# Kernel optimization log

Measured on AMD Instinct MI355X. Metric: run time of the kernel, lower is better.

The kernel has to match this reference:

```python
import jax, jax.numpy as jnp
import numpy as np

N_GRAPHS = 512
NODES_PER_G = 200
EDGES_PER_G = 6400
N = N_GRAPHS * NODES_PER_G        # 102400 nodes
E = N_GRAPHS * EDGES_PER_G        # 3276800 edges
HID = 128
NCLS = 10


def _linear_params(key, fan_in, fan_out):
    # torch nn.Linear default init: U(-1/sqrt(fan_in), 1/sqrt(fan_in))
    s = 1.0 / np.sqrt(fan_in)
    kw, kb = jax.random.split(key)
    W = jax.random.uniform(kw, (fan_in, fan_out), minval=-s, maxval=s, dtype=jnp.float32)
    b = jax.random.uniform(kb, (fan_out,), minval=-s, maxval=s, dtype=jnp.float32)
    return W, b


def setup_inputs() -> dict:
    key = jax.random.key(0)
    ks = jax.random.split(key, 10)
    # edges are confined within each graph (DGL batched graph structure)
    g_off = (jnp.arange(E, dtype=jnp.int32) // EDGES_PER_G) * NODES_PER_G
    src = (g_off + jax.random.randint(ks[0], (E,), 0, NODES_PER_G)).astype(jnp.int32)
    dst = (g_off + jax.random.randint(ks[1], (E,), 0, NODES_PER_G)).astype(jnp.int32)
    W1, b1 = _linear_params(ks[2], 1, HID)
    W2, b2 = _linear_params(ks[3], HID, HID)
    Wa, ba = _linear_params(ks[4], HID, 512)
    Wb, bb = _linear_params(ks[5], 512, 1024)
    Wc, bc = _linear_params(ks[6], 1024, 1024)
    Wd, bd = _linear_params(ks[7], 1024, 512)
    We, be = _linear_params(ks[8], 512, NCLS)
    return dict(src=src, dst=dst, W1=W1, b1=b1, W2=W2, b2=b2,
                Wa=Wa, ba=ba, Wb=Wb, bb=bb, Wc=Wc, bc=bc,
                Wd=Wd, bd=bd, We=We, be=be)


def reference(src, dst, W1, b1, W2, b2, Wa, ba, Wb, bb, Wc, bc, Wd, bd, We, be):
    seg = jax.ops.segment_sum
    ones = jnp.ones((E,), jnp.float32)
    in_deg = seg(ones, dst, num_segments=N)    # [N]
    out_deg = seg(ones, src, num_segments=N)   # [N]
    # DGL GraphConv norm='both': degrees clamped to min 1
    inv_out = (1.0 / jnp.sqrt(jnp.maximum(out_deg, 1.0)))[:, None]
    inv_in = (1.0 / jnp.sqrt(jnp.maximum(in_deg, 1.0)))[:, None]

    def gconv(h, W, b):
        h = (h @ W) * inv_out                    # src-side normalize (weight applied first; same math)
        h = seg(h[src], dst, num_segments=N)     # gather + scatter-add aggregation
        return h * inv_in + b                    # dst-side normalize + bias

    h = in_deg[:, None]                          # input node features = in-degrees, [N,1]
    h = jax.nn.relu(gconv(h, W1, b1))
    h = jax.nn.relu(gconv(h, W2, b2))

    gid = jnp.arange(N, dtype=jnp.int32) // NODES_PER_G
    hg = seg(h, gid, num_segments=N_GRAPHS) / float(NODES_PER_G)  # mean readout, [G,HID]

    x = jax.nn.relu(hg @ Wa + ba)
    x = jax.nn.relu(x @ Wb + bb)
    x = jax.nn.relu(x @ Wc + bc)
    x = jax.nn.relu(x @ Wd + bd)
    return jax.nn.softmax(x @ We + be, axis=-1)  # nn.Softmax over class dim
```

## Files before the change

### kernel.cpp

```cpp
#include <hip/hip_runtime.h>
#include <stdint.h>

typedef unsigned short u16;
typedef unsigned int   u32;

#define NG   512
#define NPG  200
#define EPG  6400
#define NN   (NG*NPG)
#define NE_  (NG*EPG)
#define HID  128
#define KP   224
#define AP   232
#define ZP   136
#define RQ   64
#define QCAP 2048

__device__ __forceinline__ float bf2f(u16 b){ u32 u = ((u32)b) << 16; return __builtin_bit_cast(float, u); }
__device__ __forceinline__ u16 f2bf(float f){
    u32 u = __builtin_bit_cast(u32, f);
    u = (u + 0x7FFFu + ((u >> 16) & 1u)) >> 16;
    return (u16)u;
}

typedef __attribute__((ext_vector_type(8))) short bf16x8;
typedef __attribute__((ext_vector_type(4))) float f32x4;

enum : int {
  O_W1 = 0,        O_b1 = 128,      O_W2 = 256,      O_b2 = 16640,
  O_Wa = 16768,    O_ba = 82304,    O_Wb = 82816,    O_bb = 607104,
  O_Wc = 608128,   O_bc = 1656704,  O_Wd = 1657728,  O_bd = 2182016,
  O_We = 2182528,  O_be = 2187648,  O_END = 2187658
};

enum : int {
  T_Wa = 0,
  T_Wb = 65536,
  T_Wc = 65536 + 524288,
  T_Wd = 65536 + 524288 + 1048576,
  T_END = 65536 + 524288 + 1048576 + 524288
};

__global__ __launch_bounds__(128) void k_detect(const u16* __restrict__ w1bits,
                                                int* __restrict__ flag)
{
    __shared__ int cnt;
    const int tid = threadIdx.x;
    if (tid == 0) cnt = 0;
    __syncthreads();
    u16 u = w1bits[tid];
    int e = (u >> 7) & 0xFF;
    if (e >= 0x7F) atomicAdd(&cnt, 1);
    __syncthreads();
    if (tid == 0) *flag = (cnt > 4) ? 1 : 0;
}

struct Cvt { const void* src[14]; int off[15]; };

__global__ __launch_bounds__(256) void k_convert(Cvt c, float* __restrict__ dst,
                                                 const int* __restrict__ flag, int total)
{
    const int f = *flag;
    int i = blockIdx.x * 256 + threadIdx.x;
    if (i >= total) return;
    int t = 0;
    while (i >= c.off[t+1]) t++;
    int j = i - c.off[t];
    dst[i] = f ? ((const float*)c.src[t])[j] : bf2f(((const u16*)c.src[t])[j]);
}

__global__ __launch_bounds__(256) void k_w2t(const void* __restrict__ w2src,
                                             const float* __restrict__ w2canon,
                                             u16* __restrict__ W2T,
                                             float* __restrict__ hg,
                                             const int* __restrict__ flag)
{
    int i = blockIdx.x * 256 + threadIdx.x;
    if (i < HID*HID){
        int outc = i >> 7, inc = i & 127;
        int jsrc = inc*HID + outc;
        W2T[i] = (*flag) ? f2bf(w2canon[jsrc]) : ((const u16*)w2src)[jsrc];
    }
    #pragma unroll
    for (int k = 0; k < 4; k++){
        int j = blockIdx.x * 1024 + k*256 + threadIdx.x;
        if (j < NG*HID) hg[j] = 0.f;
    }
}

struct TD { const void* src; int coff; int logK; int N; int dst0; int dst1; };
struct TD4 { TD t[4]; };

__global__ __launch_bounds__(256) void k_wt(TD4 d, const float* __restrict__ canon,
                                            u16* __restrict__ dst,
                                            const int* __restrict__ flag, int total)
{
    const int f = *flag;
    int i = blockIdx.x * 256 + threadIdx.x;
    if (i >= total) return;
    int t = 0;
    while (i >= d.t[t].dst1) t++;
    const TD& td = d.t[t];
    int j = i - td.dst0;
    int n = j >> td.logK;
    int k = j & ((1 << td.logK) - 1);
    int srcidx = k * td.N + n;
    dst[i] = f ? f2bf(canon[td.coff + srcidx]) : ((const u16*)td.src)[srcidx];
}

__global__ __launch_bounds__(256) void k_graph_l1(
    const int* __restrict__ src, const int* __restrict__ dst,
    const float* __restrict__ W1, const float* __restrict__ b1,
    float* __restrict__ invInG, u16* __restrict__ h1sT,
    u32* __restrict__ edgeBuf, int* __restrict__ cntQ)
{
    __shared__ u16 srcL[EPG];
    __shared__ u16 dstL[EPG];
    __shared__ int degIn[NPG];
    __shared__ int degOut[NPG];
    __shared__ int qcur[4];
    __shared__ float sValL[NPG], sAgg[NPG], iiL[NPG], ioL[NPG], tL[NPG];
    __shared__ float w1L[HID], b1L[HID];

    const int g = blockIdx.x, tid = threadIdx.x;

    if (tid < NPG){ degIn[tid] = 0; degOut[tid] = 0; sAgg[tid] = 0.f; }
    if (tid < HID){ w1L[tid] = W1[tid]; b1L[tid] = b1[tid]; }
    if (tid < 4) qcur[tid] = 0;
    __syncthreads();

    const int ebase = g * EPG;
    #pragma unroll
    for (int i = 0; i < EPG/256; i++){
        int e = i*256 + tid;
        int s = src[ebase + e] - g*NPG;
        int d = dst[ebase + e] - g*NPG;
        srcL[e] = (u16)s; dstL[e] = (u16)d;
        atomicAdd(&degOut[s], 1);
        atomicAdd(&degIn[d], 1);
    }
    __syncthreads();

    if (tid < NPG){
        int din = degIn[tid], dout = degOut[tid];
        float ii = rsqrtf(fmaxf((float)din, 1.f));
        float io = rsqrtf(fmaxf((float)dout, 1.f));
        iiL[tid] = ii; ioL[tid] = io;
        sValL[tid] = (float)din * io;
        invInG[g*NPG + tid] = ii;
    }
    __syncthreads();

    #pragma unroll
    for (int i = 0; i < EPG/256; i++){
        int e = i*256 + tid;
        int s = srcL[e], d = dstL[e];
        atomicAdd(&sAgg[d], sValL[s]);
        int q = (d * 41) >> 11;
        int pos = atomicAdd(&qcur[q], 1);
        if (pos < QCAP)
            edgeBuf[((size_t)(g*4 + q))*QCAP + pos] = (u32)s | ((u32)(d - q*50) << 16);
    }
    __syncthreads();

    if (tid < 4) cntQ[g*4 + tid] = (qcur[tid] < QCAP) ? qcur[tid] : QCAP;
    if (tid < NPG) tL[tid] = sAgg[tid] * iiL[tid];
    __syncthreads();

    const size_t base = (size_t)g * HID * KP;
    #pragma unroll 4
    for (int i = 0; i < HID*KP/256; i++){
        int idx = i*256 + tid;
        int c = idx / KP, v = idx - c*KP;
        u16 o = 0;
        if (v < NPG)
            o = f2bf(fmaxf(fmaf(tL[v], w1L[c], b1L[c]), 0.f) * ioL[v]);
        h1sT[base + idx] = o;
    }
}

__global__ __launch_bounds__(256, 4) void k_fused_graph(
    const u32* __restrict__ edgeBuf, const int* __restrict__ cntQ,
    const u16* __restrict__ h1sT, const u16* __restrict__ W2T,
    const float* __restrict__ invInG, const float* __restrict__ b2,
    float* __restrict__ hg)
{
    __shared__ __align__(16) u16 AZ[RQ*AP];
    __shared__ float invInL[RQ];
    __shared__ float b2L[HID];
    __shared__ float poolL[HID];

    const int bid = blockIdx.x, tid = threadIdx.x;
    const int g = bid >> 2, q = bid & 3;
    u32* az32 = (u32*)AZ;
    uint4* az4 = (uint4*)AZ;

    #pragma unroll
    for (int i = 0; i < 8; i++){
        int idx = i*256 + tid;
        if (idx < RQ*AP/8) az4[idx] = make_uint4(0,0,0,0);
    }
    if (tid < HID){ b2L[tid] = b2[tid]; poolL[tid] = 0.f; }
    if (tid < RQ) invInL[tid] = (tid < 50) ? invInG[g*NPG + q*50 + tid] : 0.f;
    __syncthreads();

    const int cnt = cntQ[bid];
    const u32* eb = edgeBuf + (size_t)bid * QCAP;
    for (int i = tid; i < cnt; i += 256){
        u32 e = eb[i];
        int s = e & 0xFFFF, dl = e >> 16;
        int idx = dl*AP + s;
        atomicAdd(&az32[idx >> 1], 1u << (16*(idx & 1)));
    }
    __syncthreads();

    for (int i = tid; i < RQ*AP/2; i += 256){
        u32 wv = az32[i];
        if (wv)
            az32[i] = (u32)f2bf((float)(wv & 0xFFFFu)) | ((u32)f2bf((float)(wv >> 16)) << 16);
    }
    __syncthreads();

    const int w = tid >> 6, lane = tid & 63;
    const int wm = w >> 1, wn = w & 1;
    const int lr = lane & 15, quad = lane >> 4;

    f32x4 acc[2][4];
    const f32x4 fz = {0.f, 0.f, 0.f, 0.f};
    #pragma unroll
    for (int mi = 0; mi < 2; mi++)
        #pragma unroll
        for (int nt = 0; nt < 4; nt++) acc[mi][nt] = fz;

    {
        const u16* Bg = h1sT + (size_t)g * HID * KP + (size_t)(wn*64) * KP;
        bf16x8 bcur[4], bnxt[4];
        #pragma unroll
        for (int nt = 0; nt < 4; nt++)
            bcur[nt] = *(const bf16x8*)&Bg[(nt*16 + lr)*KP + quad*8];
        for (int ks = 0; ks < 7; ks++){
            if (ks < 6){
                #pragma unroll
                for (int nt = 0; nt < 4; nt++)
                    bnxt[nt] = *(const bf16x8*)&Bg[(nt*16 + lr)*KP + (ks+1)*32 + quad*8];
            }
            bf16x8 af[2];
            #pragma unroll
            for (int mi = 0; mi < 2; mi++)
                af[mi] = *(const bf16x8*)&AZ[((wm*2 + mi)*16 + lr)*AP + ks*32 + quad*8];
            #pragma unroll
            for (int mi = 0; mi < 2; mi++)
                #pragma unroll
                for (int nt = 0; nt < 4; nt++)
                    acc[mi][nt] = __builtin_amdgcn_mfma_f32_16x16x32_bf16(
                        af[mi], bcur[nt], acc[mi][nt], 0, 0, 0);
            #pragma unroll
            for (int nt = 0; nt < 4; nt++) bcur[nt] = bnxt[nt];
        }
    }
    __syncthreads();

    #pragma unroll
    for (int mi = 0; mi < 2; mi++)
        #pragma unroll
        for (int nt = 0; nt < 4; nt++)
            #pragma unroll
            for (int r = 0; r < 4; r++){
                int v = (wm*2 + mi)*16 + quad*4 + r;
                int c = wn*64 + nt*16 + lr;
                AZ[v*ZP + c] = f2bf(acc[mi][nt][r]);
            }
    __syncthreads();

    #pragma unroll
    for (int mi = 0; mi < 2; mi++)
        #pragma unroll
        for (int nt = 0; nt < 4; nt++) acc[mi][nt] = fz;
    {
        const u16* Wg = W2T + (size_t)(wn*64) * HID;
        bf16x8 bcur[4], bnxt[4];
        #pragma unroll
        for (int nt = 0; nt < 4; nt++)
            bcur[nt] = *(const bf16x8*)&Wg[(nt*16 + lr)*HID + quad*8];
        for (int ks = 0; ks < 4; ks++){
            if (ks < 3){
                #pragma unroll
                for (int nt = 0; nt < 4; nt++)
                    bnxt[nt] = *(const bf16x8*)&Wg[(nt*16 + lr)*HID + (ks+1)*32 + quad*8];
            }
            bf16x8 af[2];
            #pragma unroll
            for (int mi = 0; mi < 2; mi++)
                af[mi] = *(const bf16x8*)&AZ[((wm*2 + mi)*16 + lr)*ZP + ks*32 + quad*8];
            #pragma unroll
            for (int mi = 0; mi < 2; mi++)
                #pragma unroll
                for (int nt = 0; nt < 4; nt++)
                    acc[mi][nt] = __builtin_amdgcn_mfma_f32_16x16x32_bf16(
                        af[mi], bcur[nt], acc[mi][nt], 0, 0, 0);
            #pragma unroll
            for (int nt = 0; nt < 4; nt++) bcur[nt] = bnxt[nt];
        }
    }

    #pragma unroll
    for (int mi = 0; mi < 2; mi++)
        #pragma unroll
        for (int nt = 0; nt < 4; nt++){
            int c = wn*64 + nt*16 + lr;
            float s = 0.f;
            #pragma unroll
            for (int r = 0; r < 4; r++){
                int v = (wm*2 + mi)*16 + quad*4 + r;
                if (v < 50)
                    s += fmaxf(fmaf(acc[mi][nt][r], invInL[v], b2L[c]), 0.f);
            }
            atomicAdd(&poolL[c], s);
        }
    __syncthreads();
    if (tid < HID) atomicAdd(&hg[(size_t)g*HID + tid], poolL[tid] * (1.f / NPG));
}

template<int K, bool AF32>
__global__ __launch_bounds__(512) void k_mlp3(
    const void* __restrict__ Ahi_, const u16* __restrict__ Alo,
    const u16* __restrict__ WT, const float* __restrict__ bias,
    u16* __restrict__ Ohi, u16* __restrict__ Olo, int Nc)
{
    __shared__ float red[32][68];

    const int tid = threadIdx.x;
    const int w = tid >> 6, lane = tid & 63;
    const int kz = w >> 2, wm = (w >> 1) & 1, wn = w & 1;
    const int lr = lane & 15, quad = lane >> 4;
    const int row0 = blockIdx.x * 32, col0 = blockIdx.y * 64;
    const int m = row0 + wm*16 + lr;
    constexpr int KH = K / 2;
    const int k0 = kz * KH;

    const float* Af = (const float*)Ahi_;
    const u16*   Ah = (const u16*)Ahi_;

    const f32x4 fz = {0.f, 0.f, 0.f, 0.f};
    f32x4 acc[2] = {fz, fz};

    #pragma unroll
    for (int ks = 0; ks < KH/32; ks++){
        const int kk = k0 + ks*32 + quad*8;
        bf16x8 ahi, alo;
        if constexpr (AF32){
            float xs[8];
            *(float4*)&xs[0] = *(const float4*)&Af[(size_t)m*K + kk];
            *(float4*)&xs[4] = *(const float4*)&Af[(size_t)m*K + kk + 4];
            #pragma unroll
            for (int j = 0; j < 8; j++){
                u16 hh = f2bf(xs[j]);
                ahi[j] = (short)hh;
                alo[j] = (short)f2bf(xs[j] - bf2f(hh));
            }
        } else {
            ahi = *(const bf16x8*)&Ah[(size_t)m*K + kk];
            alo = *(const bf16x8*)&Alo[(size_t)m*K + kk];
        }
        #pragma unroll
        for (int nt = 0; nt < 2; nt++){
            int n = col0 + wn*32 + nt*16 + lr;
            bf16x8 b = *(const bf16x8*)&WT[(size_t)n*K + kk];
            acc[nt] = __builtin_amdgcn_mfma_f32_16x16x32_bf16(ahi, b, acc[nt], 0, 0, 0);
            acc[nt] = __builtin_amdgcn_mfma_f32_16x16x32_bf16(alo, b, acc[nt], 0, 0, 0);
        }
    }

    if (kz == 1){
        #pragma unroll
        for (int nt = 0; nt < 2; nt++)
            #pragma unroll
            for (int r = 0; r < 4; r++)
                red[wm*16 + quad*4 + r][wn*32 + nt*16 + lr] = acc[nt][r];
    }
    __syncthreads();
    if (kz == 0){
        #pragma unroll
        for (int nt = 0; nt < 2; nt++)
            #pragma unroll
            for (int r = 0; r < 4; r++){
                int rr = wm*16 + quad*4 + r;
                int cc = wn*32 + nt*16 + lr;
                float v = acc[nt][r] + red[rr][cc] + bias[col0 + cc];
                v = fmaxf(v, 0.f);
                u16 hh = f2bf(v);
                size_t go = (size_t)(row0 + rr) * Nc + col0 + cc;
                Ohi[go] = hh;
                Olo[go] = f2bf(v - bf2f(hh));
            }
    }
}

__global__ __launch_bounds__(64) void k_head(
    const u16* __restrict__ Xhi, const u16* __restrict__ Xlo,
    const float* __restrict__ We, const float* __restrict__ be,
    void* __restrict__ out, const int* __restrict__ flag)
{
    const int g = blockIdx.x, lane = threadIdx.x;
    float part[10];
    #pragma unroll
    for (int c = 0; c < 10; c++) part[c] = 0.f;
    for (int k = lane; k < 512; k += 64){
        float x = bf2f(Xhi[(size_t)g*512 + k]) + bf2f(Xlo[(size_t)g*512 + k]);
        #pragma unroll
        for (int c = 0; c < 10; c++) part[c] = fmaf(x, We[k*10 + c], part[c]);
    }
    #pragma unroll
    for (int c = 0; c < 10; c++){
        float v = part[c];
        for (int off = 32; off > 0; off >>= 1) v += __shfl_down(v, off);
        part[c] = v;
    }
    if (lane == 0){
        const int f = *flag;
        #pragma unroll
        for (int c = 0; c < 10; c++) part[c] += be[c];
        float m = part[0];
        #pragma unroll
        for (int c = 1; c < 10; c++) m = fmaxf(m, part[c]);
        float e[10], s = 0.f;
        #pragma unroll
        for (int c = 0; c < 10; c++){ e[c] = __expf(part[c] - m); s += e[c]; }
        float inv = 1.f / s;
        #pragma unroll
        for (int c = 0; c < 10; c++){
            float p = e[c] * inv;
            if (f) ((float*)out)[g*10 + c] = p;
            else   ((u16*)out)[g*10 + c]  = f2bf(p);
        }
    }
}

extern "C" void kernel_launch(void* const* d_in, const int* in_sizes, int n_in,
                              void* d_out, int out_size, void* d_ws, size_t ws_size,
                              hipStream_t stream)
{
    const int* src = (const int*)d_in[0];
    const int* dst = (const int*)d_in[1];

    char* ws = (char*)d_ws;
    size_t o = 0;
    int*   flag     = (int*)  (ws + o); o += 16;
    float* wcanon   = (float*)(ws + o); o += ((size_t)O_END * 4 + 15) & ~(size_t)15;
    u16*   W2T      = (u16*)  (ws + o); o += (size_t)HID * HID * 2;
    u16*   WTa      = (u16*)  (ws + o); o += ((size_t)T_END * 2 + 15) & ~(size_t)15;
    float* invIn    = (float*)(ws + o); o += (size_t)NN * 4;
    u32*   edgeBuf  = (u32*)  (ws + o); o += (size_t)NG * 4 * QCAP * 4;
    int*   cntQ     = (int*)  (ws + o); o += (size_t)NG * 4 * 4;
    u16*   h1sT     = (u16*)  (ws + o); o += (size_t)NG * HID * KP * 2;
    float* hg       = (float*)(ws + o); o += (size_t)NG * HID * 4;
    u16*   X1hi     = (u16*)  (ws + o); o += (size_t)NG * 512 * 2;
    u16*   X1lo     = (u16*)  (ws + o); o += (size_t)NG * 512 * 2;
    u16*   X2hi     = (u16*)  (ws + o); o += (size_t)NG * 1024 * 2;
    u16*   X2lo     = (u16*)  (ws + o); o += (size_t)NG * 1024 * 2;
    u16*   X3hi     = (u16*)  (ws + o); o += (size_t)NG * 1024 * 2;
    u16*   X3lo     = (u16*)  (ws + o); o += (size_t)NG * 1024 * 2;
    u16*   X4hi     = (u16*)  (ws + o); o += (size_t)NG * 512 * 2;
    u16*   X4lo     = (u16*)  (ws + o); o += (size_t)NG * 512 * 2;
    (void)ws_size; (void)in_sizes; (void)n_in; (void)out_size;

    k_detect<<<dim3(1), dim3(128), 0, stream>>>((const u16*)d_in[2], flag);

    Cvt cv;
    const int offs[15] = {O_W1,O_b1,O_W2,O_b2,O_Wa,O_ba,O_Wb,O_bb,O_Wc,O_bc,O_Wd,O_bd,O_We,O_be,O_END};
    for (int i = 0; i < 14; i++){ cv.src[i] = d_in[2 + i]; cv.off[i] = offs[i]; }
    cv.off[14] = offs[14];
    k_convert<<<dim3((O_END + 255)/256), dim3(256), 0, stream>>>(cv, wcanon, flag, O_END);
    k_w2t<<<dim3(64), dim3(256), 0, stream>>>(d_in[4], wcanon + O_W2, W2T, hg, flag);

    TD4 td;
    td.t[0] = { d_in[6],  O_Wa, 7,  512,  T_Wa, T_Wb };
    td.t[1] = { d_in[8],  O_Wb, 9,  1024, T_Wb, T_Wc };
    td.t[2] = { d_in[10], O_Wc, 10, 1024, T_Wc, T_Wd };
    td.t[3] = { d_in[12], O_Wd, 10, 512,  T_Wd, T_END };
    k_wt<<<dim3((T_END + 255)/256), dim3(256), 0, stream>>>(td, wcanon, WTa, flag, T_END);

    const float *W1 = wcanon+O_W1, *b1 = wcanon+O_b1, *b2 = wcanon+O_b2;
    const float *ba = wcanon+O_ba, *bb = wcanon+O_bb, *bc = wcanon+O_bc, *bd = wcanon+O_bd;
    const float *We = wcanon+O_We, *be = wcanon+O_be;

    k_graph_l1<<<dim3(NG), dim3(256), 0, stream>>>(
        src, dst, W1, b1, invIn, h1sT, edgeBuf, cntQ);

    k_fused_graph<<<dim3(NG*4), dim3(256), 0, stream>>>(
        edgeBuf, cntQ, h1sT, W2T, invIn, b2, hg);

    k_mlp3<128,  true ><<<dim3(16, 8),  dim3(512), 0, stream>>>(hg,   nullptr, WTa + T_Wa, ba, X1hi, X1lo, 512);
    k_mlp3<512,  false><<<dim3(16, 16), dim3(512), 0, stream>>>(X1hi, X1lo,    WTa + T_Wb, bb, X2hi, X2lo, 1024);
    k_mlp3<1024, false><<<dim3(16, 16), dim3(512), 0, stream>>>(X2hi, X2lo,    WTa + T_Wc, bc, X3hi, X3lo, 1024);
    k_mlp3<1024, false><<<dim3(16, 8),  dim3(512), 0, stream>>>(X3hi, X3lo,    WTa + T_Wd, bd, X4hi, X4lo, 512);

    k_head<<<dim3(NG), dim3(64), 0, stream>>>(X4hi, X4lo, We, be, d_out, flag);
}
```

Measured before the change: 278.8 us.

## Replace bucketed edge queues with packed edges, remap blocks per XCD, split-K MLP

The graph layer-1 kernel now writes every edge as a packed u32 instead of bucketing edges into per-quarter queues with shared atomics and a capacity cap. The fused graph kernel instead reads all edges of its graph and keeps only those in its quarter. Block-to-graph mapping is swizzled so the four quarter-blocks of a graph land on the same XCD and can share L2 for the packed edges. The MLP kernel is restructured to split K across up to 8 waves, each computing a full 32x64 tile, reduced with LDS float atomics and written back with vectorized stores. This trades more edge reads per block for removing queue atomics and the QCAP overflow risk.

Result: slower. 325.4 us (+16.7%).

```diff
diff --git a/kernel.cpp b/kernel.cpp
--- a/kernel.cpp
+++ b/kernel.cpp
@@ -14,7 +14,6 @@
 #define AP   232
 #define ZP   136
 #define RQ   64
-#define QCAP 2048
 
 __device__ __forceinline__ float bf2f(u16 b){ u32 u = ((u32)b) << 16; return __builtin_bit_cast(float, u); }
 __device__ __forceinline__ u16 f2bf(float f){
@@ -112,13 +111,12 @@
     const int* __restrict__ src, const int* __restrict__ dst,
     const float* __restrict__ W1, const float* __restrict__ b1,
     float* __restrict__ invInG, u16* __restrict__ h1sT,
-    u32* __restrict__ edgeBuf, int* __restrict__ cntQ)
+    u32* __restrict__ pkE)
 {
     __shared__ u16 srcL[EPG];
     __shared__ u16 dstL[EPG];
     __shared__ int degIn[NPG];
     __shared__ int degOut[NPG];
-    __shared__ int qcur[4];
     __shared__ float sValL[NPG], sAgg[NPG], iiL[NPG], ioL[NPG], tL[NPG];
     __shared__ float w1L[HID], b1L[HID];
 
@@ -126,7 +124,6 @@
 
     if (tid < NPG){ degIn[tid] = 0; degOut[tid] = 0; sAgg[tid] = 0.f; }
     if (tid < HID){ w1L[tid] = W1[tid]; b1L[tid] = b1[tid]; }
-    if (tid < 4) qcur[tid] = 0;
     __syncthreads();
 
     const int ebase = g * EPG;
@@ -136,6 +133,7 @@
         int s = src[ebase + e] - g*NPG;
         int d = dst[ebase + e] - g*NPG;
         srcL[e] = (u16)s; dstL[e] = (u16)d;
+        pkE[ebase + e] = (u32)s | ((u32)d << 16);
         atomicAdd(&degOut[s], 1);
         atomicAdd(&degIn[d], 1);
     }
@@ -154,16 +152,10 @@
     #pragma unroll
     for (int i = 0; i < EPG/256; i++){
         int e = i*256 + tid;
-        int s = srcL[e], d = dstL[e];
-        atomicAdd(&sAgg[d], sValL[s]);
-        int q = (d * 41) >> 11;
-        int pos = atomicAdd(&qcur[q], 1);
-        if (pos < QCAP)
-            edgeBuf[((size_t)(g*4 + q))*QCAP + pos] = (u32)s | ((u32)(d - q*50) << 16);
-    }
-    __syncthreads();
-
-    if (tid < 4) cntQ[g*4 + tid] = (qcur[tid] < QCAP) ? qcur[tid] : QCAP;
+        atomicAdd(&sAgg[dstL[e]], sValL[srcL[e]]);
+    }
+    __syncthreads();
+
     if (tid < NPG) tL[tid] = sAgg[tid] * iiL[tid];
     __syncthreads();
 
@@ -180,7 +172,7 @@
 }
 
 __global__ __launch_bounds__(256, 4) void k_fused_graph(
-    const u32* __restrict__ edgeBuf, const int* __restrict__ cntQ,
+    const u32* __restrict__ pkE,
     const u16* __restrict__ h1sT, const u16* __restrict__ W2T,
     const float* __restrict__ invInG, const float* __restrict__ b2,
     float* __restrict__ hg)
@@ -191,7 +183,9 @@
     __shared__ float poolL[HID];
 
     const int bid = blockIdx.x, tid = threadIdx.x;
-    const int g = bid >> 2, q = bid & 3;
+    const int xcd = bid & 7, slot = bid >> 3;
+    const int g = (slot >> 2) * 8 + xcd;
+    const int q = slot & 3;
     u32* az32 = (u32*)AZ;
     uint4* az4 = (uint4*)AZ;
 
@@ -204,13 +198,16 @@
     if (tid < RQ) invInL[tid] = (tid < 50) ? invInG[g*NPG + q*50 + tid] : 0.f;
     __syncthreads();
 
-    const int cnt = cntQ[bid];
-    const u32* eb = edgeBuf + (size_t)bid * QCAP;
-    for (int i = tid; i < cnt; i += 256){
-        u32 e = eb[i];
-        int s = e & 0xFFFF, dl = e >> 16;
-        int idx = dl*AP + s;
-        atomicAdd(&az32[idx >> 1], 1u << (16*(idx & 1)));
+    const u32* eb = pkE + (size_t)g * EPG;
+    #pragma unroll
+    for (int i = 0; i < EPG/256; i++){
+        u32 e = eb[i*256 + tid];
+        int s = e & 0xFFFF, d = e >> 16;
+        int qe = (d * 41) >> 11;
+        if (qe == q){
+            int idx = (d - q*50)*AP + s;
+            atomicAdd(&az32[idx >> 1], 1u << (16*(idx & 1)));
+        }
     }
     __syncthreads();
 
@@ -322,77 +319,95 @@
 }
 
 template<int K, bool AF32>
-__global__ __launch_bounds__(512) void k_mlp3(
+__global__ __launch_bounds__(512) void k_mlp4(
     const void* __restrict__ Ahi_, const u16* __restrict__ Alo,
     const u16* __restrict__ WT, const float* __restrict__ bias,
     u16* __restrict__ Ohi, u16* __restrict__ Olo, int Nc)
 {
-    __shared__ float red[32][68];
+    constexpr int KW = (K >= 256) ? 8 : 4;
+    constexpr int NT = (KW == 8) ? 4 : 2;
+    constexpr int ITERS = K / KW / 32;
+    __shared__ __align__(16) float accC[32][68];
 
     const int tid = threadIdx.x;
     const int w = tid >> 6, lane = tid & 63;
-    const int kz = w >> 2, wm = (w >> 1) & 1, wn = w & 1;
+    const int kz = w % KW;
+    const int ntb = (KW == 8) ? 0 : (w >> 2) * 2;
     const int lr = lane & 15, quad = lane >> 4;
     const int row0 = blockIdx.x * 32, col0 = blockIdx.y * 64;
-    const int m = row0 + wm*16 + lr;
-    constexpr int KH = K / 2;
-    const int k0 = kz * KH;
+
+    for (int i = tid; i < 32*68/4; i += 512)
+        ((float4*)&accC[0][0])[i] = make_float4(0.f, 0.f, 0.f, 0.f);
+    __syncthreads();
 
     const float* Af = (const float*)Ahi_;
     const u16*   Ah = (const u16*)Ahi_;
 
     const f32x4 fz = {0.f, 0.f, 0.f, 0.f};
-    f32x4 acc[2] = {fz, fz};
-
-    #pragma unroll
-    for (int ks = 0; ks < KH/32; ks++){
-        const int kk = k0 + ks*32 + quad*8;
-        bf16x8 ahi, alo;
-        if constexpr (AF32){
-            float xs[8];
-            *(float4*)&xs[0] = *(const float4*)&Af[(size_t)m*K + kk];
-            *(float4*)&xs[4] = *(const float4*)&Af[(size_t)m*K + kk + 4];
-            #pragma unroll
-            for (int j = 0; j < 8; j++){
-                u16 hh = f2bf(xs[j]);
-                ahi[j] = (short)hh;
-                alo[j] = (short)f2bf(xs[j] - bf2f(hh));
+    f32x4 acc[2][NT];
+    #pragma unroll
+    for (int mi = 0; mi < 2; mi++)
+        #pragma unroll
+        for (int nt = 0; nt < NT; nt++) acc[mi][nt] = fz;
+
+    #pragma unroll
+    for (int it = 0; it < ITERS; it++){
+        const int kk = kz*(K/KW) + it*32 + quad*8;
+        bf16x8 ahi[2], alo[2];
+        #pragma unroll
+        for (int mi = 0; mi < 2; mi++){
+            const int m = row0 + mi*16 + lr;
+            if constexpr (AF32){
+                float xs[8];
+                *(float4*)&xs[0] = *(const float4*)&Af[(size_t)m*K + kk];
+                *(float4*)&xs[4] = *(const float4*)&Af[(size_t)m*K + kk + 4];
+                #pragma unroll
+                for (int j = 0; j < 8; j++){
+                    u16 hh = f2bf(xs[j]);
+                    ahi[mi][j] = (short)hh;
+                    alo[mi][j] = (short)f2bf(xs[j] - bf2f(hh));
+                }
+            } else {
+                ahi[mi] = *(const bf16x8*)&Ah[(size_t)m*K + kk];
+                alo[mi] = *(const bf16x8*)&Alo[(size_t)m*K + kk];
             }
-        } else {
-            ahi = *(const bf16x8*)&Ah[(size_t)m*K + kk];
-            alo = *(const bf16x8*)&Alo[(size_t)m*K + kk];
-        }
-        #pragma unroll
-        for (int nt = 0; nt < 2; nt++){
-            int n = col0 + wn*32 + nt*16 + lr;
+        }
+        #pragma unroll
+        for (int nt = 0; nt < NT; nt++){
+            const int n = col0 + (ntb + nt)*16 + lr;
             bf16x8 b = *(const bf16x8*)&WT[(size_t)n*K + kk];
-            acc[nt] = __builtin_amdgcn_mfma_f32_16x16x32_bf16(ahi, b, acc[nt], 0, 0, 0);
-            acc[nt] = __builtin_amdgcn_mfma_f32_16x16x32_bf16(alo, b, acc[nt], 0, 0, 0);
-        }
-    }
-
-    if (kz == 1){
-        #pragma unroll
-        for (int nt = 0; nt < 2; nt++)
+            #pragma unroll
+            for (int mi = 0; mi < 2; mi++){
+                acc[mi][nt] = __builtin_amdgcn_mfma_f32_16x16x32_bf16(ahi[mi], b, acc[mi][nt], 0, 0, 0);
+                acc[mi][nt] = __builtin_amdgcn_mfma_f32_16x16x32_bf16(alo[mi], b, acc[mi][nt], 0, 0, 0);
+            }
+        }
+    }
+
+    #pragma unroll
+    for (int mi = 0; mi < 2; mi++)
+        #pragma unroll
+        for (int nt = 0; nt < NT; nt++)
             #pragma unroll
             for (int r = 0; r < 4; r++)
-                red[wm*16 + quad*4 + r][wn*32 + nt*16 + lr] = acc[nt][r];
-    }
-    __syncthreads();
-    if (kz == 0){
-        #pragma unroll
-        for (int nt = 0; nt < 2; nt++)
-            #pragma unroll
-            for (int r = 0; r < 4; r++){
-                int rr = wm*16 + quad*4 + r;
-                int cc = wn*32 + nt*16 + lr;
-                float v = acc[nt][r] + red[rr][cc] + bias[col0 + cc];
-                v = fmaxf(v, 0.f);
-                u16 hh = f2bf(v);
-                size_t go = (size_t)(row0 + rr) * Nc + col0 + cc;
-                Ohi[go] = hh;
-                Olo[go] = f2bf(v - bf2f(hh));
-            }
+                atomicAdd(&accC[mi*16 + quad*4 + r][(ntb + nt)*16 + lr], acc[mi][nt][r]);
+    __syncthreads();
+
+    {
+        const int rr = tid >> 4;
+        const int cc = (tid & 15) * 4;
+        float4 v = *(const float4*)&accC[rr][cc];
+        float4 b = *(const float4*)&bias[col0 + cc];
+        float t0 = fmaxf(v.x + b.x, 0.f), t1 = fmaxf(v.y + b.y, 0.f);
+        float t2 = fmaxf(v.z + b.z, 0.f), t3 = fmaxf(v.w + b.w, 0.f);
+        u16 h0 = f2bf(t0), h1 = f2bf(t1), h2 = f2bf(t2), h3 = f2bf(t3);
+        u16 l0 = f2bf(t0 - bf2f(h0)), l1 = f2bf(t1 - bf2f(h1));
+        u16 l2 = f2bf(t2 - bf2f(h2)), l3 = f2bf(t3 - bf2f(h3));
+        const size_t go = (size_t)(row0 + rr) * Nc + col0 + cc;
+        uint2 hv = { (u32)h0 | ((u32)h1 << 16), (u32)h2 | ((u32)h3 << 16) };
+        uint2 lv = { (u32)l0 | ((u32)l1 << 16), (u32)l2 | ((u32)l3 << 16) };
+        *(uint2*)&Ohi[go] = hv;
+        *(uint2*)&Olo[go] = lv;
     }
 }
 
@@ -450,8 +465,7 @@
     u16*   W2T      = (u16*)  (ws + o); o += (size_t)HID * HID * 2;
     u16*   WTa      = (u16*)  (ws + o); o += ((size_t)T_END * 2 + 15) & ~(size_t)15;
     float* invIn    = (float*)(ws + o); o += (size_t)NN * 4;
-    u32*   edgeBuf  = (u32*)  (ws + o); o += (size_t)NG * 4 * QCAP * 4;
-    int*   cntQ     = (int*)  (ws + o); o += (size_t)NG * 4 * 4;
+    u32*   pkE      = (u32*)  (ws + o); o += (size_t)NE_ * 4;
     u16*   h1sT     = (u16*)  (ws + o); o += (size_t)NG * HID * KP * 2;
     float* hg       = (float*)(ws + o); o += (size_t)NG * HID * 4;
     u16*   X1hi     = (u16*)  (ws + o); o += (size_t)NG * 512 * 2;
@@ -485,15 +499,15 @@
     const float *We = wcanon+O_We, *be = wcanon+O_be;
 
     k_graph_l1<<<dim3(NG), dim3(256), 0, stream>>>(
-        src, dst, W1, b1, invIn, h1sT, edgeBuf, cntQ);
+        src, dst, W1, b1, invIn, h1sT, pkE);
 
     k_fused_graph<<<dim3(NG*4), dim3(256), 0, stream>>>(
-        edgeBuf, cntQ, h1sT, W2T, invIn, b2, hg);
-
-    k_mlp3<128,  true ><<<dim3(16, 8),  dim3(512), 0, stream>>>(hg,   nullptr, WTa + T_Wa, ba, X1hi, X1lo, 512);
-    k_mlp3<512,  false><<<dim3(16, 16), dim3(512), 0, stream>>>(X1hi, X1lo,    WTa + T_Wb, bb, X2hi, X2lo, 1024);
-    k_mlp3<1024, false><<<dim3(16, 16), dim3(512), 0, stream>>>(X2hi, X2lo,    WTa + T_Wc, bc, X3hi, X3lo, 1024);
-    k_mlp3<1024, false><<<dim3(16, 8),  dim3(512), 0, stream>>>(X3hi, X3lo,    WTa + T_Wd, bd, X4hi, X4lo, 512);
+        pkE, h1sT, W2T, invIn, b2, hg);
+
+    k_mlp4<128,  true ><<<dim3(16, 8),  dim3(512), 0, stream>>>(hg,   nullptr, WTa + T_Wa, ba, X1hi, X1lo, 512);
+    k_mlp4<512,  false><<<dim3(16, 16), dim3(512), 0, stream>>>(X1hi, X1lo,    WTa + T_Wb, bb, X2hi, X2lo, 1024);
+    k_mlp4<1024, false><<<dim3(16, 16), dim3(512), 0, stream>>>(X2hi, X2lo,    WTa + T_Wc, bc, X3hi, X3lo, 1024);
+    k_mlp4<1024, false><<<dim3(16, 8),  dim3(512), 0, stream>>>(X3hi, X3lo,    WTa + T_Wd, bd, X4hi, X4lo, 512);
 
     k_head<<<dim3(NG), dim3(64), 0, stream>>>(X4hi, X4lo, We, be, d_out, flag);
 }
```
